# Kernel optimization log

Hardware: AMD Instinct MI355X
Metric: run time of the kernel (lower is better)

## Reference

```python
import jax, jax.numpy as jnp
import numpy as np

N_COARSE = 100_000
M_FINE = 4 * N_COARSE
GRID = 128
C_IN, C_HID, C_OUT = 32, 64, 32
K3 = 27   # 3x3x3 neighborhood
K2 = 8    # 2x2x2 transposed-conv offsets


def setup_inputs() -> dict:
    rng = np.random.default_rng(0)
    # --- sparse coarse grid: N unique voxels in GRID^3 ---
    lin = np.sort(rng.choice(GRID ** 3, size=N_COARSE, replace=False))
    cx, cy, cz = lin // (GRID * GRID), (lin // GRID) % GRID, lin % GRID
    coords = np.stack([cx, cy, cz], 1).astype(np.int64)
    # --- rulebook: neighbor index per voxel per 3^3 offset (sentinel = N) ---
    offs = np.array([(dx, dy, dz) for dx in (-1, 0, 1) for dy in (-1, 0, 1) for dz in (-1, 0, 1)])
    nbr = np.full((N_COARSE, K3), N_COARSE, np.int32)
    for k in range(K3):
        nc = coords + offs[k]
        valid = ((nc >= 0) & (nc < GRID)).all(1)
        nlin = nc[:, 0] * GRID * GRID + nc[:, 1] * GRID + nc[:, 2]
        pos = np.clip(np.searchsorted(lin, nlin), 0, N_COARSE - 1)
        found = valid & (lin[pos] == nlin)
        nbr[found, k] = pos[found].astype(np.int32)
    # --- fine grid: 4 distinct children (of 8) per coarse voxel ---
    child = np.argsort(rng.random((N_COARSE, K2)), axis=1)[:, :4].astype(np.int32)
    parent_idx = np.repeat(np.arange(N_COARSE, dtype=np.int32), 4)
    offset_idx = child.reshape(-1)

    key = jax.random.key(0)
    ks = jax.random.split(key, 16)
    nrm = lambda k, sh, fan: (jax.random.normal(k, sh, jnp.float32) / np.sqrt(fan)).astype(jnp.float32)
    return {
        "feats_in": jax.random.normal(ks[0], (N_COARSE, C_IN), jnp.float32),
        "x_up_feats": jax.random.normal(ks[1], (M_FINE, C_OUT), jnp.float32),
        "nbr_idx": jnp.asarray(nbr),
        "parent_idx": jnp.asarray(parent_idx),
        "offset_idx": jnp.asarray(offset_idx),
        "W_enc1": nrm(ks[2], (K3, C_IN, C_HID), K3 * C_IN),
        "b_enc1": jnp.zeros((C_HID,), jnp.float32),
        "W_enc2": nrm(ks[3], (K3, C_HID, C_HID), K3 * C_HID),
        "b_enc2": jnp.zeros((C_HID,), jnp.float32),
        "W_enc3": nrm(ks[4], (K3, C_HID, C_HID), K3 * C_HID),
        "b_enc3": jnp.zeros((C_HID,), jnp.float32),
        "W_t": nrm(ks[5], (K2, C_HID, C_HID), C_HID),
        "b_t": jnp.zeros((C_HID,), jnp.float32),
        "W_d1": nrm(ks[6], (C_HID, C_HID), C_HID),
        "b_d1": jnp.zeros((C_HID,), jnp.float32),
        "W_d2": nrm(ks[7], (C_HID, C_OUT), C_HID),
        "b_d2": jnp.zeros((C_OUT,), jnp.float32),
    }


def _sparse_conv3(x, nbr, W, b):
    """3x3x3 stride-1 sparse conv: gather neighbors, per-offset matmul, accumulate.
    x: [N,Cin], nbr: [N,27] (sentinel N -> zero feature), W: [27,Cin,Cout]."""
    xp = jnp.concatenate([x, jnp.zeros((1, x.shape[1]), x.dtype)], 0)  # sentinel row
    acc = jnp.broadcast_to(b, (x.shape[0], W.shape[-1]))
    for k in range(W.shape[0]):  # fixed 27-way structural loop
        acc = acc + xp[nbr[:, k]] @ W[k]
    return acc


def _t_conv2(x, parent_idx, offset_idx, W, b):
    """2x2x2 stride-2 transposed sparse conv onto a given fine grid.
    x: [N,C], parent_idx: [M] (sentinel N), offset_idx: [M] in [0,8)."""
    xp = jnp.concatenate([x, jnp.zeros((1, x.shape[1]), x.dtype)], 0)
    g = xp[parent_idx]  # [M,C]
    out = jnp.broadcast_to(b, (g.shape[0], W.shape[-1]))
    for k in range(W.shape[0]):  # fixed 8-way structural loop
        out = out + jnp.where((offset_idx == k)[:, None], g @ W[k], 0.0)
    return out


def reference(feats_in, x_up_feats, nbr_idx, parent_idx, offset_idx,
              W_enc1, b_enc1, W_enc2, b_enc2, W_enc3, b_enc3,
              W_t, b_t, W_d1, b_d1, W_d2, b_d2):
    # encoder: (conv -> dropout[eval: identity] -> relu) x 3
    x = jax.nn.relu(_sparse_conv3(feats_in, nbr_idx, W_enc1, b_enc1))
    x = jax.nn.relu(_sparse_conv3(x, nbr_idx, W_enc2, b_enc2))
    x = jax.nn.relu(_sparse_conv3(x, nbr_idx, W_enc3, b_enc3))
    # transposed upsample conv onto x_upsample's grid
    x = _t_conv2(x, parent_idx, offset_idx, W_t, b_t)
    # decoder: relu -> 1x1 conv -> relu -> 1x1 conv, then residual add
    x = jax.nn.relu(x) @ W_d1 + b_d1
    x = jax.nn.relu(x) @ W_d2 + b_d2
    return x + x_up_feats
```

## Files before the change

### kernel.cpp

```cpp
#include <hip/hip_runtime.h>
#include <hip/hip_bf16.h>

#define NC 100000
#define MF 400000
#define K3 27

typedef __bf16 bf16_t;
typedef bf16_t bf16x8 __attribute__((ext_vector_type(8)));
typedef float  f32x4  __attribute__((ext_vector_type(4)));

#define O_E1 0
#define O_E2 55296
#define O_E3 165888
#define O_T  276480
#define O_D1 309248
#define O_D2 313344
#define W_TOTAL 315392

__device__ __align__(16) bf16_t g_w[W_TOTAL];
__device__ __align__(16) bf16_t g_x0[(size_t)NC * 32];
__device__ __align__(16) bf16_t g_x1[(size_t)NC * 64];
__device__ __align__(16) bf16_t g_x2[(size_t)NC * 64];
__device__ int g_nbrT[(size_t)K3 * NC];

static __device__ __forceinline__ bf16x8 zero8() {
    bf16x8 v;
#pragma unroll
    for (int i = 0; i < 8; ++i) v[i] = (bf16_t)0.0f;
    return v;
}

__global__ __launch_bounds__(256) void prep_k(
    const float* __restrict__ W_e1, const float* __restrict__ W_e2,
    const float* __restrict__ W_e3, const float* __restrict__ W_t,
    const float* __restrict__ W_d1, const float* __restrict__ W_d2,
    const float* __restrict__ feats, const int* __restrict__ nbr)
{
    int b = blockIdx.x;
    if (b < 154) {
        int tid = b * 256 + threadIdx.x;
        int lane = tid & 63;
        int f = tid >> 6;
        const float* src; int doff, nt, nc, fb;
        if      (f < 108) { src = W_e1; doff = O_E1; nt = 4; nc = 1; fb = 0;   }
        else if (f < 324) { src = W_e2; doff = O_E2; nt = 4; nc = 2; fb = 108; }
        else if (f < 540) { src = W_e3; doff = O_E3; nt = 4; nc = 2; fb = 324; }
        else if (f < 604) { src = W_t;  doff = O_T;  nt = 4; nc = 2; fb = 540; }
        else if (f < 612) { src = W_d1; doff = O_D1; nt = 4; nc = 2; fb = 604; }
        else              { src = W_d2; doff = O_D2; nt = 2; nc = 2; fb = 612; }
        int lf = f - fb;
        int t  = lf % nt;
        int c  = (lf / nt) % nc;
        int ko = lf / (nt * nc);
        int Cin = nc * 32, Cout = nt * 16;
        int n  = t * 16 + (lane & 15);
        int kb = c * 32 + (lane >> 4) * 8;
        bf16x8 tmp;
#pragma unroll
        for (int j = 0; j < 8; ++j)
            tmp[j] = (bf16_t)src[((size_t)ko * Cin + (kb + j)) * Cout + n];
        *(bf16x8*)(g_w + doff + (size_t)lf * 512 + lane * 8) = tmp;
    } else if (b < 1717) {
        int i = (b - 154) * 256 + threadIdx.x;
        if (i < NC * 32 / 8) {
            const f32x4* p = (const f32x4*)(feats + (size_t)i * 8);
            f32x4 lo = p[0], hi = p[1];
            bf16x8 v;
#pragma unroll
            for (int j = 0; j < 4; ++j) { v[j] = (bf16_t)lo[j]; v[j + 4] = (bf16_t)hi[j]; }
            *(bf16x8*)(g_x0 + (size_t)i * 8) = v;
        }
    } else {
        int r = (b - 1717) * 256 + threadIdx.x;
        if (r < NC) {
#pragma unroll
            for (int k = 0; k < K3; ++k)
                g_nbrT[(size_t)k * NC + r] = nbr[(size_t)r * K3 + k];
        }
    }
}

#define TS 72

#define CSTEP(KO, P) do {                                                      \
    if ((KO) + 1 < K3) {                                                       \
               \
        const bf16x8* s_ = (const bf16x8*)(wsrc + (size_t)((KO) + 1) * CH * 2048); \
        bf16x8* d_ = (bf16x8*)bB[(P) ^ 1];                                     \
        _Pragma("unroll")                                                      \
        for (int i_ = 0; i_ < CH * 2; ++i_)                                    \
            d_[i_ * 128 + tid] = s_[i_ * 128 + tid];                           \
                         \
        _Pragma("unroll")                                                      \
        for (int c_ = 0; c_ < CH; ++c_)                                        \
            _Pragma("unroll")                                                  \
            for (int mt_ = 0; mt_ < 2; ++mt_) {                                \
                int ii_ = idxbuf[(P) ^ 1][mt_];                                \
                bool va_ = (unsigned)ii_ < (unsigned)NC;                       \
                int ss_ = va_ ? ii_ : 0;                                       \
                bf16x8 a_ = *(const bf16x8*)(xb + (size_t)ss_ * CIN + c_ * 32 + q * 8); \
                if (!va_) a_ = zero8();                                        \
                abuf[(P) ^ 1][c_][mt_] = a_;                                   \
            }                                                                  \
    }                                                                          \
    if ((KO) + 2 < K3) {                                                       \
                     \
        _Pragma("unroll")                                                      \
        for (int mt_ = 0; mt_ < 2; ++mt_) {                                    \
            int r_ = base + mt_ * 16 + cl;                                     \
            idxbuf[P][mt_] = (r_ < NC) ? g_nbrT[(size_t)((KO) + 2) * NC + r_] : NC; \
        }                                                                      \
    }                                                                          \
                           \
    _Pragma("unroll")                                                          \
    for (int c_ = 0; c_ < CH; ++c_) {                                          \
        bf16x8 bfr_[4];                                                        \
        _Pragma("unroll")                                                      \
        for (int t_ = 0; t_ < 4; ++t_)                                         \
            bfr_[t_] = *(const bf16x8*)&bB[P][(c_ * 4 + t_) * 512 + lane * 8]; \
        _Pragma("unroll")                                                      \
        for (int mt_ = 0; mt_ < 2; ++mt_)                                      \
            _Pragma("unroll")                                                  \
            for (int t_ = 0; t_ < 4; ++t_)                                     \
                acc[mt_][t_] = __builtin_amdgcn_mfma_f32_16x16x32_bf16(        \
                    abuf[P][c_][mt_], bfr_[t_], acc[mt_][t_], 0, 0, 0);        \
    }                                                                          \
    __syncthreads();                                                           \
} while (0)

template <int CH>
__global__ __launch_bounds__(128, 2) void conv_k(
    int w_off,
    const float* __restrict__ bias,
    int src_sel, int dst_sel)
{
    constexpr int CIN = CH * 32;
    const bf16_t* xb = (src_sel == 0) ? g_x0 : (src_sel == 1 ? g_x1 : g_x2);
    bf16_t* y = (dst_sel == 1) ? g_x1 : g_x2;
    const bf16_t* wsrc = g_w + w_off;

    __shared__ __align__(16) bf16_t bB[2][4096];
    int tid = threadIdx.x;
    int wv = tid >> 6, lane = tid & 63;
    int cl = lane & 15, q = lane >> 4;

    int per = gridDim.x >> 3;
    int blk = (blockIdx.x & 7) * per + (blockIdx.x >> 3);
    int base = blk * 64 + wv * 32;

    {
        const bf16x8* s = (const bf16x8*)wsrc;
        bf16x8* d = (bf16x8*)bB[0];
#pragma unroll
        for (int i = 0; i < CH * 2; ++i) d[i * 128 + tid] = s[i * 128 + tid];
    }

    int idxbuf[2][2];
    bf16x8 abuf[2][CH][2];
#pragma unroll
    for (int mt = 0; mt < 2; ++mt) {
        int r = base + mt * 16 + cl;
        idxbuf[0][mt] = (r < NC) ? g_nbrT[(size_t)0 * NC + r] : NC;
    }
#pragma unroll
    for (int c = 0; c < CH; ++c)
#pragma unroll
        for (int mt = 0; mt < 2; ++mt) {
            int ii = idxbuf[0][mt];
            bool va = (unsigned)ii < (unsigned)NC;
            int ss = va ? ii : 0;
            bf16x8 a = *(const bf16x8*)(xb + (size_t)ss * CIN + c * 32 + q * 8);
            if (!va) a = zero8();
            abuf[0][c][mt] = a;
        }
#pragma unroll
    for (int mt = 0; mt < 2; ++mt) {
        int r = base + mt * 16 + cl;
        idxbuf[1][mt] = (r < NC) ? g_nbrT[(size_t)1 * NC + r] : NC;
    }

    f32x4 acc[2][4];
#pragma unroll
    for (int t = 0; t < 4; ++t) {
        float b = bias[t * 16 + cl];
#pragma unroll
        for (int mt = 0; mt < 2; ++mt) acc[mt][t] = (f32x4){b, b, b, b};
    }
    __syncthreads();

    for (int ko = 0; ko < K3 - 1; ko += 2) {
        CSTEP(ko, 0);
        CSTEP(ko + 1, 1);
    }
    CSTEP(K3 - 1, 0);

    bf16_t* tb = ((bf16_t*)bB) + wv * 2304;
#pragma unroll
    for (int mt2 = 0; mt2 < 2; ++mt2)
#pragma unroll
        for (int t = 0; t < 4; ++t)
#pragma unroll
            for (int r = 0; r < 4; ++r) {
                float v = acc[mt2][t][r];
                v = v > 0.0f ? v : 0.0f;
                tb[(mt2 * 16 + q * 4 + r) * TS + t * 16 + cl] = (bf16_t)v;
            }
#pragma unroll
    for (int i = 0; i < 4; ++i) {
        int rl = i * 8 + (lane >> 3);
        int c8 = (lane & 7) * 8;
        bf16x8 v8 = *(const bf16x8*)&tb[rl * TS + c8];
        int orow = base + rl;
        if (orow < NC)
            *(bf16x8*)(y + (size_t)orow * 64 + c8) = v8;
    }
}

#define HS 72
__global__ __launch_bounds__(128) void tconv_dec_k(
    const int*   __restrict__ offs,
    const float* __restrict__ b_t,
    const float* __restrict__ b_d1,
    const float* __restrict__ b_d2,
    const float* __restrict__ x_up,
    float*       __restrict__ out)
{
    __shared__ __align__(16) bf16_t h_lds[2][64 * HS];
    __shared__ __align__(16) int off_lds[2][64];
    int wv = threadIdx.x >> 6, lane = threadIdx.x & 63;
    int cl = lane & 15, q = lane >> 4;
    int per = gridDim.x >> 3;
    int blk = (blockIdx.x & 7) * per + (blockIdx.x >> 3);
    int p0 = (blk * 2 + wv) * 16;
    int fbase = p0 * 4;

    {
        int fi = fbase + lane;
        off_lds[wv][lane] = (fi < MF) ? offs[fi] : 0;
    }
    int code[4];
#pragma unroll
    for (int r = 0; r < 4; ++r) {
        int4 o = *(const int4*)&off_lds[wv][(q * 4 + r) * 4];
        code[r] = (1 << (4 * o.x)) | (2 << (4 * o.y)) |
                  (3 << (4 * o.z)) | (4 << (4 * o.w));
    }

    bool pv = (p0 + cl) < NC;
    size_t xrow = (size_t)(pv ? p0 + cl : 0) * 64;
    bf16x8 ax[2];
#pragma unroll
    for (int c = 0; c < 2; ++c) {
        bf16x8 t8 = *(const bf16x8*)(g_x1 + xrow + c * 32 + q * 8);
        ax[c] = pv ? t8 : zero8();
    }

    const bf16_t* wt = g_w + O_T;
#pragma unroll
    for (int k = 0; k < 8; ++k) {
        f32x4 acc[4];
#pragma unroll
        for (int t = 0; t < 4; ++t) {
            float b = b_t[t * 16 + cl];
            acc[t] = (f32x4){b, b, b, b};
        }
#pragma unroll
        for (int c = 0; c < 2; ++c) {
            const bf16_t* wb = wt + ((size_t)(k * 2 + c) * 4) * 512 + lane * 8;
#pragma unroll
            for (int t = 0; t < 4; ++t) {
                bf16x8 b = *(const bf16x8*)(wb + t * 512);
                acc[t] = __builtin_amdgcn_mfma_f32_16x16x32_bf16(ax[c], b, acc[t], 0, 0, 0);
            }
        }
#pragma unroll
        for (int r = 0; r < 4; ++r) {
            int nib = (code[r] >> (4 * k)) & 0xF;
            if (nib) {
                int fl = (((q * 4 + r) * 4) + (nib - 1)) & 63;
#pragma unroll
                for (int t = 0; t < 4; ++t) {
                    float v = acc[t][r];
                    v = v > 0.0f ? v : 0.0f;
                    h_lds[wv][fl * HS + t * 16 + cl] = (bf16_t)v;
                }
            }
        }
    }

    bf16x8 a1[4][2];
#pragma unroll
    for (int mt = 0; mt < 4; ++mt)
#pragma unroll
        for (int c = 0; c < 2; ++c)
            a1[mt][c] = *(const bf16x8*)&h_lds[wv][(mt * 16 + cl) * HS + c * 32 + q * 8];

#pragma unroll
    for (int mt = 0; mt < 4; ++mt) {
        f32x4 acc2[4];
#pragma unroll
        for (int t = 0; t < 4; ++t) {
            float b = b_d1[t * 16 + cl];
            acc2[t] = (f32x4){b, b, b, b};
        }
#pragma unroll
        for (int c = 0; c < 2; ++c)
#pragma unroll
            for (int t = 0; t < 4; ++t) {
                bf16x8 b = *(const bf16x8*)(g_w + O_D1 + (size_t)(c * 4 + t) * 512 + lane * 8);
                acc2[t] = __builtin_amdgcn_mfma_f32_16x16x32_bf16(a1[mt][c], b, acc2[t], 0, 0, 0);
            }
#pragma unroll
        for (int t = 0; t < 4; ++t)
#pragma unroll
            for (int r = 0; r < 4; ++r) {
                float v = acc2[t][r];
                v = v > 0.0f ? v : 0.0f;
                h_lds[wv][(mt * 16 + q * 4 + r) * HS + t * 16 + cl] = (bf16_t)v;
            }
    }

    float* fW = (float*)h_lds[wv];
#pragma unroll
    for (int mt = 0; mt < 4; ++mt) {
        bf16x8 a2[2];
#pragma unroll
        for (int c = 0; c < 2; ++c)
            a2[c] = *(const bf16x8*)&h_lds[wv][(mt * 16 + cl) * HS + c * 32 + q * 8];
        f32x4 acc3[2];
#pragma unroll
        for (int t = 0; t < 2; ++t) {
            float b = b_d2[t * 16 + cl];
            acc3[t] = (f32x4){b, b, b, b};
        }
#pragma unroll
        for (int c = 0; c < 2; ++c)
#pragma unroll
            for (int t = 0; t < 2; ++t) {
                bf16x8 b = *(const bf16x8*)(g_w + O_D2 + (size_t)(c * 2 + t) * 512 + lane * 8);
                acc3[t] = __builtin_amdgcn_mfma_f32_16x16x32_bf16(a2[c], b, acc3[t], 0, 0, 0);
            }
#pragma unroll
        for (int t = 0; t < 2; ++t)
#pragma unroll
            for (int r = 0; r < 4; ++r)
                fW[(mt * 16 + q * 4 + r) * 36 + t * 16 + cl] = acc3[t][r];
    }

#pragma unroll
    for (int i = 0; i < 8; ++i) {
        int rl = i * 8 + (lane >> 3);
        int c4 = (lane & 7) * 4;
        int fg = fbase + rl;
        if (fg < MF) {
            f32x4 xv = *(const f32x4*)(x_up + (size_t)fg * 32 + c4);
            f32x4 v = *(const f32x4*)&fW[rl * 36 + c4];
            v += xv;
            *(f32x4*)(out + (size_t)fg * 32 + c4) = v;
        }
    }
}

extern "C" void kernel_launch(void* const* d_in, const int* in_sizes, int n_in,
                              void* d_out, int out_size, void* d_ws, size_t ws_size,
                              hipStream_t stream) {
    const float* feats  = (const float*)d_in[0];
    const float* x_up   = (const float*)d_in[1];
    const int*   nbr    = (const int*)d_in[2];
    const int*   offs   = (const int*)d_in[4];
    const float* W_e1 = (const float*)d_in[5];
    const float* b_e1 = (const float*)d_in[6];
    const float* W_e2 = (const float*)d_in[7];
    const float* b_e2 = (const float*)d_in[8];
    const float* W_e3 = (const float*)d_in[9];
    const float* b_e3 = (const float*)d_in[10];
    const float* W_t  = (const float*)d_in[11];
    const float* b_t  = (const float*)d_in[12];
    const float* W_d1 = (const float*)d_in[13];
    const float* b_d1 = (const float*)d_in[14];
    const float* W_d2 = (const float*)d_in[15];
    const float* b_d2 = (const float*)d_in[16];
    float* out = (float*)d_out;

    prep_k<<<2108, 256, 0, stream>>>(W_e1, W_e2, W_e3, W_t, W_d1, W_d2, feats, nbr);

    conv_k<1><<<1568, 128, 0, stream>>>(O_E1, b_e1, 0, 1);
    conv_k<2><<<1568, 128, 0, stream>>>(O_E2, b_e2, 1, 2);
    conv_k<2><<<1568, 128, 0, stream>>>(O_E3, b_e3, 2, 1);

    tconv_dec_k<<<3128, 128, 0, stream>>>(offs, b_t, b_d1, b_d2, x_up, out);
}
```

Before: 294.0 us.

## Split conv kernel offsets across waves and read weights straight from global

The sparse conv kernel now splits the 27 neighbor offsets between two waves for the same 32 rows, then merges the partial sums through LDS. Weights come straight from global memory (cache-resident) into registers instead of being staged in double-buffered LDS, which removes the per-offset __syncthreads. The grid doubles and occupancy is raised to 3 blocks per SM. The risks are more global/L2 weight traffic per wave and a reduction step at the end.

```diff
diff --git a/kernel.cpp b/kernel.cpp
--- a/kernel.cpp
+++ b/kernel.cpp
@@ -82,14 +82,18 @@
 
 #define TS 72
 
-#define CSTEP(KO, P) do {                                                      \
-    if ((KO) + 1 < K3) {                                                       \
-               \
-        const bf16x8* s_ = (const bf16x8*)(wsrc + (size_t)((KO) + 1) * CH * 2048); \
-        bf16x8* d_ = (bf16x8*)bB[(P) ^ 1];                                     \
+#define KSTEP(KO, P) do {                                                      \
+         \
+    bf16x8 bfr[CH][4];                                                         \
+    {                                                                          \
+        const bf16_t* wb_ = wsrc + (size_t)(KO) * CH * 2048 + lane * 8;        \
         _Pragma("unroll")                                                      \
-        for (int i_ = 0; i_ < CH * 2; ++i_)                                    \
-            d_[i_ * 128 + tid] = s_[i_ * 128 + tid];                           \
+        for (int c_ = 0; c_ < CH; ++c_)                                        \
+            _Pragma("unroll")                                                  \
+            for (int t_ = 0; t_ < 4; ++t_)                                     \
+                bfr[c_][t_] = *(const bf16x8*)(wb_ + (size_t)(c_ * 4 + t_) * 512); \
+    }                                                                          \
+    if ((KO) + 1 < kend) {                                                     \
                          \
         _Pragma("unroll")                                                      \
         for (int c_ = 0; c_ < CH; ++c_)                                        \
@@ -103,7 +107,7 @@
                 abuf[(P) ^ 1][c_][mt_] = a_;                                   \
             }                                                                  \
     }                                                                          \
-    if ((KO) + 2 < K3) {                                                       \
+    if ((KO) + 2 < kend) {                                                     \
                      \
         _Pragma("unroll")                                                      \
         for (int mt_ = 0; mt_ < 2; ++mt_) {                                    \
@@ -111,25 +115,19 @@
             idxbuf[P][mt_] = (r_ < NC) ? g_nbrT[(size_t)((KO) + 2) * NC + r_] : NC; \
         }                                                                      \
     }                                                                          \
-                           \
+                                       \
     _Pragma("unroll")                                                          \
-    for (int c_ = 0; c_ < CH; ++c_) {                                          \
-        bf16x8 bfr_[4];                                                        \
-        _Pragma("unroll")                                                      \
-        for (int t_ = 0; t_ < 4; ++t_)                                         \
-            bfr_[t_] = *(const bf16x8*)&bB[P][(c_ * 4 + t_) * 512 + lane * 8]; \
+    for (int c_ = 0; c_ < CH; ++c_)                                            \
         _Pragma("unroll")                                                      \
         for (int mt_ = 0; mt_ < 2; ++mt_)                                      \
             _Pragma("unroll")                                                  \
             for (int t_ = 0; t_ < 4; ++t_)                                     \
                 acc[mt_][t_] = __builtin_amdgcn_mfma_f32_16x16x32_bf16(        \
-                    abuf[P][c_][mt_], bfr_[t_], acc[mt_][t_], 0, 0, 0);        \
-    }                                                                          \
-    __syncthreads();                                                           \
+                    abuf[P][c_][mt_], bfr[c_][t_], acc[mt_][t_], 0, 0, 0);     \
 } while (0)
 
 template <int CH>
-__global__ __launch_bounds__(128, 2) void conv_k(
+__global__ __launch_bounds__(128, 3) void conv_k(
     int w_off,
     const float* __restrict__ bias,
     int src_sel, int dst_sel)
@@ -139,28 +137,27 @@
     bf16_t* y = (dst_sel == 1) ? g_x1 : g_x2;
     const bf16_t* wsrc = g_w + w_off;
 
-    __shared__ __align__(16) bf16_t bB[2][4096];
+    __shared__ __align__(16) float  red[2][1280];
+    __shared__ __align__(16) bf16_t tb2[2][16 * TS];
+
     int tid = threadIdx.x;
     int wv = tid >> 6, lane = tid & 63;
     int cl = lane & 15, q = lane >> 4;
 
     int per = gridDim.x >> 3;
     int blk = (blockIdx.x & 7) * per + (blockIdx.x >> 3);
-    int base = blk * 64 + wv * 32;
-
-    {
-        const bf16x8* s = (const bf16x8*)wsrc;
-        bf16x8* d = (bf16x8*)bB[0];
-#pragma unroll
-        for (int i = 0; i < CH * 2; ++i) d[i * 128 + tid] = s[i * 128 + tid];
-    }
+    int base = blk * 32;
+
+    int kbeg = wv ? 13 : 0;
+    int kend = wv ? K3 : 13;
 
     int idxbuf[2][2];
     bf16x8 abuf[2][CH][2];
+
 #pragma unroll
     for (int mt = 0; mt < 2; ++mt) {
         int r = base + mt * 16 + cl;
-        idxbuf[0][mt] = (r < NC) ? g_nbrT[(size_t)0 * NC + r] : NC;
+        idxbuf[0][mt] = (r < NC) ? g_nbrT[(size_t)kbeg * NC + r] : NC;
     }
 #pragma unroll
     for (int c = 0; c < CH; ++c)
@@ -176,41 +173,55 @@
 #pragma unroll
     for (int mt = 0; mt < 2; ++mt) {
         int r = base + mt * 16 + cl;
-        idxbuf[1][mt] = (r < NC) ? g_nbrT[(size_t)1 * NC + r] : NC;
+        idxbuf[1][mt] = (r < NC) ? g_nbrT[(size_t)(kbeg + 1) * NC + r] : NC;
     }
 
     f32x4 acc[2][4];
 #pragma unroll
     for (int t = 0; t < 4; ++t) {
-        float b = bias[t * 16 + cl];
+        float b = wv ? 0.0f : bias[t * 16 + cl];
 #pragma unroll
         for (int mt = 0; mt < 2; ++mt) acc[mt][t] = (f32x4){b, b, b, b};
     }
+
+    int ko = kbeg;
+    for (; ko + 1 < kend; ko += 2) {
+        KSTEP(ko, 0);
+        KSTEP(ko + 1, 1);
+    }
+    if (ko < kend) KSTEP(ko, 0);
+
+    {
+        float* rb = red[wv];
+        const int emt = 1 - wv;
+#pragma unroll
+        for (int t = 0; t < 4; ++t)
+            *(f32x4*)&rb[lane * 20 + t * 4] = acc[emt][t];
+    }
     __syncthreads();
-
-    for (int ko = 0; ko < K3 - 1; ko += 2) {
-        CSTEP(ko, 0);
-        CSTEP(ko + 1, 1);
-    }
-    CSTEP(K3 - 1, 0);
-
-    bf16_t* tb = ((bf16_t*)bB) + wv * 2304;
-#pragma unroll
-    for (int mt2 = 0; mt2 < 2; ++mt2)
+    {
+        const float* rb = red[1 - wv];
+        const int omt = wv;
 #pragma unroll
         for (int t = 0; t < 4; ++t)
-#pragma unroll
-            for (int r = 0; r < 4; ++r) {
-                float v = acc[mt2][t][r];
-                v = v > 0.0f ? v : 0.0f;
-                tb[(mt2 * 16 + q * 4 + r) * TS + t * 16 + cl] = (bf16_t)v;
-            }
-#pragma unroll
-    for (int i = 0; i < 4; ++i) {
+            acc[omt][t] += *(const f32x4*)&rb[lane * 20 + t * 4];
+    }
+
+    bf16_t* tb = tb2[wv];
+#pragma unroll
+    for (int t = 0; t < 4; ++t)
+#pragma unroll
+        for (int r = 0; r < 4; ++r) {
+            float v = acc[wv][t][r];
+            v = v > 0.0f ? v : 0.0f;
+            tb[(q * 4 + r) * TS + t * 16 + cl] = (bf16_t)v;
+        }
+#pragma unroll
+    for (int i = 0; i < 2; ++i) {
         int rl = i * 8 + (lane >> 3);
         int c8 = (lane & 7) * 8;
         bf16x8 v8 = *(const bf16x8*)&tb[rl * TS + c8];
-        int orow = base + rl;
+        int orow = base + wv * 16 + rl;
         if (orow < NC)
             *(bf16x8*)(y + (size_t)orow * 64 + c8) = v8;
     }
@@ -384,9 +395,9 @@
 
     prep_k<<<2108, 256, 0, stream>>>(W_e1, W_e2, W_e3, W_t, W_d1, W_d2, feats, nbr);
 
-    conv_k<1><<<1568, 128, 0, stream>>>(O_E1, b_e1, 0, 1);
-    conv_k<2><<<1568, 128, 0, stream>>>(O_E2, b_e2, 1, 2);
-    conv_k<2><<<1568, 128, 0, stream>>>(O_E3, b_e3, 2, 1);
+    conv_k<1><<<3128, 128, 0, stream>>>(O_E1, b_e1, 0, 1);
+    conv_k<2><<<3128, 128, 0, stream>>>(O_E2, b_e2, 1, 2);
+    conv_k<2><<<3128, 128, 0, stream>>>(O_E3, b_e3, 2, 1);
 
     tconv_dec_k<<<3128, 128, 0, stream>>>(offs, b_t, b_d1, b_d2, x_up, out);
 }
```

Result: slower. 345.9 us (+17.7%).

## Stage conv weights via direct global-to-LDS loads with explicit vmcnt pipelining

Applied to the files above, without the earlier changes.

Copies of per-offset weight tiles into shared memory now use global_load_lds, so the data no longer passes through VGPRs. The gather/MFMA step is split into separate stage, gather, index-load and MFMA macros. The full __syncthreads is replaced with an s_waitcnt vmcnt(N) plus s_barrier, which waits only for the weight stage while the feature gathers and index loads for later steps stay in flight. Scheduling barriers pin the instruction order, and the final offsets are peeled. This depends on in-order vmcnt retirement and on the hand-counted wait numbers being exact; a wrong count would be a race.

```diff
diff --git a/kernel.cpp b/kernel.cpp
--- a/kernel.cpp
+++ b/kernel.cpp
@@ -82,36 +82,42 @@
 
 #define TS 72
 
-#define CSTEP(KO, P) do {                                                      \
-    if ((KO) + 1 < K3) {                                                       \
-               \
-        const bf16x8* s_ = (const bf16x8*)(wsrc + (size_t)((KO) + 1) * CH * 2048); \
-        bf16x8* d_ = (bf16x8*)bB[(P) ^ 1];                                     \
-        _Pragma("unroll")                                                      \
-        for (int i_ = 0; i_ < CH * 2; ++i_)                                    \
-            d_[i_ * 128 + tid] = s_[i_ * 128 + tid];                           \
-                         \
-        _Pragma("unroll")                                                      \
-        for (int c_ = 0; c_ < CH; ++c_)                                        \
-            _Pragma("unroll")                                                  \
-            for (int mt_ = 0; mt_ < 2; ++mt_) {                                \
-                int ii_ = idxbuf[(P) ^ 1][mt_];                                \
-                bool va_ = (unsigned)ii_ < (unsigned)NC;                       \
-                int ss_ = va_ ? ii_ : 0;                                       \
-                bf16x8 a_ = *(const bf16x8*)(xb + (size_t)ss_ * CIN + c_ * 32 + q * 8); \
-                if (!va_) a_ = zero8();                                        \
-                abuf[(P) ^ 1][c_][mt_] = a_;                                   \
-            }                                                                  \
+#define STAGE_B(KO, P) do {                                                    \
+    _Pragma("unroll")                                                          \
+    for (int i_ = 0; i_ < CH * 2; ++i_) {                                      \
+        const bf16_t* gs_ = wsrc + (size_t)(KO) * CH * 2048                    \
+                          + wv * (CH * 1024) + i_ * 512 + lane * 8;            \
+        __builtin_amdgcn_global_load_lds(                                      \
+            (const __attribute__((address_space(1))) void*)gs_,                \
+            (__attribute__((address_space(3))) void*)                          \
+                (&bB[P][wv * (CH * 1024) + i_ * 512 + lane * 8]),              \
+            16, 0, 0);                                                         \
     }                                                                          \
-    if ((KO) + 2 < K3) {                                                       \
-                     \
+} while (0)
+
+#define GATHER_A(P) do {                                                       \
+    _Pragma("unroll")                                                          \
+    for (int c_ = 0; c_ < CH; ++c_)                                            \
         _Pragma("unroll")                                                      \
         for (int mt_ = 0; mt_ < 2; ++mt_) {                                    \
-            int r_ = base + mt_ * 16 + cl;                                     \
-            idxbuf[P][mt_] = (r_ < NC) ? g_nbrT[(size_t)((KO) + 2) * NC + r_] : NC; \
+            int ii_ = idxbuf[P][mt_];                                          \
+            bool va_ = (unsigned)ii_ < (unsigned)NC;                           \
+            int ss_ = va_ ? ii_ : 0;                                           \
+            bf16x8 a_ = *(const bf16x8*)(xb + (size_t)ss_ * CIN + c_ * 32 + q * 8); \
+            if (!va_) a_ = zero8();                                            \
+            abuf[P][c_][mt_] = a_;                                             \
         }                                                                      \
+} while (0)
+
+#define LOAD_IDX(KO, P) do {                                                   \
+    _Pragma("unroll")                                                          \
+    for (int mt_ = 0; mt_ < 2; ++mt_) {                                        \
+        int r_ = base + mt_ * 16 + cl;                                         \
+        idxbuf[P][mt_] = (r_ < NC) ? g_nbrT[(size_t)(KO) * NC + r_] : NC;      \
     }                                                                          \
-                           \
+} while (0)
+
+#define MFMA_KO(P) do {                                                        \
     _Pragma("unroll")                                                          \
     for (int c_ = 0; c_ < CH; ++c_) {                                          \
         bf16x8 bfr_[4];                                                        \
@@ -125,7 +131,27 @@
                 acc[mt_][t_] = __builtin_amdgcn_mfma_f32_16x16x32_bf16(        \
                     abuf[P][c_][mt_], bfr_[t_], acc[mt_][t_], 0, 0, 0);        \
     }                                                                          \
-    __syncthreads();                                                           \
+} while (0)
+
+#define CSTEP_FULL(KO, P) do {                                                 \
+    STAGE_B((KO) + 1, (P) ^ 1);                                                \
+    __builtin_amdgcn_sched_barrier(0);         \
+    GATHER_A((P) ^ 1);                                                         \
+    LOAD_IDX((KO) + 2, P);                                                     \
+    MFMA_KO(P);                                                                \
+    asm volatile("s_waitcnt vmcnt(%0)\n\ts_barrier"                            \
+                 :: "i"(CH * 2 + 2) : "memory");                               \
+    __builtin_amdgcn_sched_barrier(0);                     \
+} while (0)
+
+#define CSTEP_PEN(KO, P) do {                \
+    STAGE_B((KO) + 1, (P) ^ 1);                                                \
+    __builtin_amdgcn_sched_barrier(0);                                         \
+    GATHER_A((P) ^ 1);                                                         \
+    MFMA_KO(P);                                                                \
+    asm volatile("s_waitcnt vmcnt(%0)\n\ts_barrier"                            \
+                 :: "i"(CH * 2) : "memory");                                   \
+    __builtin_amdgcn_sched_barrier(0);                                         \
 } while (0)
 
 template <int CH>
@@ -148,36 +174,13 @@
     int blk = (blockIdx.x & 7) * per + (blockIdx.x >> 3);
     int base = blk * 64 + wv * 32;
 
-    {
-        const bf16x8* s = (const bf16x8*)wsrc;
-        bf16x8* d = (bf16x8*)bB[0];
-#pragma unroll
-        for (int i = 0; i < CH * 2; ++i) d[i * 128 + tid] = s[i * 128 + tid];
-    }
-
     int idxbuf[2][2];
     bf16x8 abuf[2][CH][2];
-#pragma unroll
-    for (int mt = 0; mt < 2; ++mt) {
-        int r = base + mt * 16 + cl;
-        idxbuf[0][mt] = (r < NC) ? g_nbrT[(size_t)0 * NC + r] : NC;
-    }
-#pragma unroll
-    for (int c = 0; c < CH; ++c)
-#pragma unroll
-        for (int mt = 0; mt < 2; ++mt) {
-            int ii = idxbuf[0][mt];
-            bool va = (unsigned)ii < (unsigned)NC;
-            int ss = va ? ii : 0;
-            bf16x8 a = *(const bf16x8*)(xb + (size_t)ss * CIN + c * 32 + q * 8);
-            if (!va) a = zero8();
-            abuf[0][c][mt] = a;
-        }
-#pragma unroll
-    for (int mt = 0; mt < 2; ++mt) {
-        int r = base + mt * 16 + cl;
-        idxbuf[1][mt] = (r < NC) ? g_nbrT[(size_t)1 * NC + r] : NC;
-    }
+
+    LOAD_IDX(0, 0);
+    GATHER_A(0);
+    LOAD_IDX(1, 1);
+    STAGE_B(0, 0);
 
     f32x4 acc[2][4];
 #pragma unroll
@@ -188,11 +191,14 @@
     }
     __syncthreads();
 
-    for (int ko = 0; ko < K3 - 1; ko += 2) {
-        CSTEP(ko, 0);
-        CSTEP(ko + 1, 1);
-    }
-    CSTEP(K3 - 1, 0);
+    for (int ko = 0; ko < 24; ko += 2) {
+        CSTEP_FULL(ko, 0);
+        CSTEP_FULL(ko + 1, 1);
+    }
+    CSTEP_FULL(24, 0);
+    CSTEP_PEN(25, 1);
+    MFMA_KO(0);
+    __syncthreads();
 
     bf16_t* tb = ((bf16_t*)bB) + wv * 2304;
 #pragma unroll
```

Measured after the change: 285.1 us. 3.0% less time.
